# Performance work log

Hardware: AMD Instinct MI355X
Metric: run time of the kernel (lower is better)

## Reference

```python
import jax, jax.numpy as jnp
import numpy as np

NUM_HEADS = 32
NUM_KV_HEADS = 8
HEAD_DIM = 128
SEQ = 2048
MAX_SLOTS = 4096
SCALE = float(1.0 / np.sqrt(HEAD_DIM))  # attn_scale
G = NUM_HEADS // NUM_KV_HEADS  # num_queries_per_kv


def setup_inputs() -> dict:
    key = jax.random.key(0)
    k1, k2, k3 = jax.random.split(key, 3)
    q = jax.random.normal(k1, (SEQ, NUM_HEADS, HEAD_DIM), dtype=jnp.float32)
    k = jax.random.normal(k2, (SEQ, NUM_KV_HEADS, HEAD_DIM), dtype=jnp.float32)
    v = jax.random.normal(k3, (SEQ, NUM_KV_HEADS, HEAD_DIM), dtype=jnp.float32)
    k_cache = jnp.zeros((MAX_SLOTS, NUM_KV_HEADS, HEAD_DIM), dtype=jnp.float32)
    v_cache = jnp.zeros((MAX_SLOTS, NUM_KV_HEADS, HEAD_DIM), dtype=jnp.float32)
    slot_mapping = jnp.arange(SEQ, dtype=jnp.int64)  # contiguous block_table slots
    return {"q": q, "k": k, "v": v, "k_cache": k_cache, "v_cache": v_cache,
            "slot_mapping": slot_mapping}


def reference(q, k, v, k_cache, v_cache, slot_mapping):
    # prefill: scatter-write new K/V into the paged cache (self.k_cache[slot_mapping] = k)
    kc = k_cache.at[slot_mapping].set(k)
    vc = v_cache.at[slot_mapping].set(v)
    # gather K/V back from the cache via slot mapping (paged gather pattern)
    k_attn = kc[slot_mapping]  # (S, Hkv, D) == k since slots are unique
    v_attn = vc[slot_mapping]
    # GQA: repeat_interleave kv heads to match query heads
    kr = jnp.repeat(k_attn, G, axis=1)  # (S, H, D)
    vr = jnp.repeat(v_attn, G, axis=1)
    # scores: (H, Sq, Sk), naive full materialization as in the original
    scores = jnp.einsum('qhd,khd->hqk', q, kr) * SCALE
    sq, sk = q.shape[0], k_attn.shape[0]
    mask = jnp.tril(jnp.ones((sq, sk), dtype=bool))  # causal (num_query_tokens > 1)
    scores = jnp.where(mask[None, :, :], scores, -jnp.inf)
    weights = jax.nn.softmax(scores, axis=-1)
    out = jnp.einsum('hqk,khd->qhd', weights, vr)  # (S, H, D)
    return out
```

## Files before the change

### kernel.cpp

```cpp
#include <hip/hip_runtime.h>
#include <hip/hip_bf16.h>

#define SEQ 2048
#define QSTR 4096
#define CSCALE 0.1275174364688796f

typedef __attribute__((ext_vector_type(8)))  short short8;
typedef __attribute__((ext_vector_type(4)))  float f32x4;
typedef __attribute__((ext_vector_type(16))) float f32x16;

union PF8 { unsigned u[4]; short8 s; };

__device__ __forceinline__ unsigned short f2bf(float f) {
    union { __hip_bfloat16 b; unsigned short u; } cv;
    cv.b = __float2bfloat16(f);
    return cv.u;
}

__device__ __forceinline__ void gload16(const unsigned short* g, unsigned short* l) {
    __builtin_amdgcn_global_load_lds(
        (const __attribute__((address_space(1))) void*)g,
        (__attribute__((address_space(3))) void*)l, 16, 0, 0);
}

__global__ void prep_k(const float* __restrict__ Kg, unsigned short* __restrict__ Kb) {
    int gi = blockIdx.x * 256 + threadIdx.x;
    int kv = gi >> 8;
    int rem = gi & 255;
    int hk = rem >> 5;
    int d4 = rem & 31;
    f32x4 k4 = *(const f32x4*)(Kg + ((size_t)kv * 8 + hk) * 128 + 4 * d4);
    ushort4 u = make_ushort4(f2bf(k4[0]), f2bf(k4[1]), f2bf(k4[2]), f2bf(k4[3]));
    *(ushort4*)(Kb + ((size_t)hk * SEQ + kv) * 128 + 4 * d4) = u;
}

__global__ void prep_v(const float* __restrict__ Vg, unsigned short* __restrict__ Vtb) {
    const int hk  = blockIdx.x >> 5;
    const int kvb = blockIdx.x & 31;
    __shared__ unsigned short T[128][72];
    const int t = threadIdx.x;
    #pragma unroll
    for (int i = 0; i < 8; ++i) {
        int idx = t + 256 * i;
        int r = idx >> 5, d4 = idx & 31;
        f32x4 v = *(const f32x4*)(Vg + ((size_t)(kvb * 64 + r) * 8 + hk) * 128 + 4 * d4);
        T[4 * d4 + 0][r] = f2bf(v[0]);
        T[4 * d4 + 1][r] = f2bf(v[1]);
        T[4 * d4 + 2][r] = f2bf(v[2]);
        T[4 * d4 + 3][r] = f2bf(v[3]);
    }
    __syncthreads();
    #pragma unroll
    for (int i = 0; i < 8; ++i) {
        int idx = t + 256 * i;
        int d = idx >> 4, c4 = idx & 15;
        ushort4 u = *(ushort4*)&T[d][4 * c4];
        *(ushort4*)(Vtb + ((size_t)hk * 128 + d) * SEQ + kvb * 64 + 4 * c4) = u;
    }
}

__launch_bounds__(512, 2)
__global__ void attn_fwd(const float* __restrict__ Qg,
                         const unsigned short* __restrict__ Kb,
                         const unsigned short* __restrict__ Vtb,
                         float* __restrict__ Og) {
    const int bid = blockIdx.x;
    const int pr  = bid >> 5;
    const int h   = bid & 31;
    const int hk  = h >> 2;
    const int QBb = 15 - pr;
    const int QBa = pr;
    const int nsB = QBb + 1;

    const int tid  = threadIdx.x;
    const int w    = tid >> 6;
    const int wq   = w & 3;
    const int wk   = w >> 2;
    const int lane = tid & 63;
    const int q5   = lane & 31;
    const int t5   = lane >> 5;

    __shared__ __align__(16) unsigned char smem[150016];
    typedef unsigned short TileT[128][128];
    TileT* Ks = (TileT*)smem;
    TileT* Vt = (TileT*)(smem + 65536);
    float* mlm = (float*)(smem + 131072);
    float* mll = (float*)(smem + 132096);
    float (*Ot)[132] = (float(*)[132])(smem + 133120);

    short8 qf[8];
    auto LOADQ = [&](int QB) __attribute__((always_inline)) {
        const float* qp = Qg + (size_t)(QB * 128 + 32 * wq + q5) * QSTR + h * 128 + 8 * t5;
        #pragma unroll
        for (int st = 0; st < 8; ++st) {
            f32x4 a = *(const f32x4*)(qp + 16 * st);
            f32x4 b = *(const f32x4*)(qp + 16 * st + 4);
            short8 f;
            f[0] = (short)f2bf(a[0] * CSCALE); f[1] = (short)f2bf(a[1] * CSCALE);
            f[2] = (short)f2bf(a[2] * CSCALE); f[3] = (short)f2bf(a[3] * CSCALE);
            f[4] = (short)f2bf(b[0] * CSCALE); f[5] = (short)f2bf(b[1] * CSCALE);
            f[6] = (short)f2bf(b[2] * CSCALE); f[7] = (short)f2bf(b[3] * CSCALE);
            qf[st] = f;
        }
    };

    auto ISSUE = [&](int kv0, int b) __attribute__((always_inline)) {
        #pragma unroll
        for (int p4 = 0; p4 < 4; ++p4) {
            int row = 16 * w + 4 * p4 + (lane >> 4);
            const unsigned short* g = Kb +
                ((size_t)hk * SEQ + kv0 + row) * 128 + 8 * ((lane & 15) ^ (row & 15));
            gload16(g, &Ks[b][16 * w + 4 * p4][0]);
        }
        #pragma unroll
        for (int p4 = 0; p4 < 4; ++p4) {
            int row16 = 16 * w + 4 * p4 + (lane >> 4);
            int hh = row16 >> 6, r = row16 & 63;
            int gg = lane & 15;
            int d  = 2 * r + (gg >> 3);
            int c  = (gg & 7) ^ (r & 7);
            const unsigned short* g = Vtb +
                ((size_t)hk * 128 + d) * SEQ + kv0 + 64 * hh + 8 * c;
            gload16(g, &Vt[b][16 * w + 4 * p4][0]);
        }
    };

    f32x16 oacc[4];
    float m, l;
    auto RESET = [&]() __attribute__((always_inline)) {
        #pragma unroll
        for (int dt = 0; dt < 4; ++dt)
            #pragma unroll
            for (int r = 0; r < 16; ++r) oacc[dt][r] = 0.f;
        m = -1e30f; l = 0.f;
    };

    auto EPI = [&](int QBp) __attribute__((always_inline)) {
        if (t5 == 0) mlm[w * 32 + q5] = m;
        asm volatile("s_waitcnt lgkmcnt(0)" ::: "memory");
        __builtin_amdgcn_sched_barrier(0);
        __builtin_amdgcn_s_barrier();
        const float mOth = mlm[(w ^ 4) * 32 + q5];
        const float M  = fmaxf(m, mOth);
        const float sc = exp2f(m - M);
        const float lp = l * sc;
        #pragma unroll
        for (int dt = 0; dt < 4; ++dt)
            #pragma unroll
            for (int r = 0; r < 16; ++r) oacc[dt][r] *= sc;
        if (t5 == 0) mll[w * 32 + q5] = lp;
        asm volatile("s_waitcnt lgkmcnt(0)" ::: "memory");
        __builtin_amdgcn_sched_barrier(0);
        __builtin_amdgcn_s_barrier();
        const float lOth = mll[(w ^ 4) * 32 + q5];

        #pragma unroll 1
        for (int tq = 0; tq < 4; ++tq) {
            if (w == tq + 4) {
                #pragma unroll
                for (int dt = 0; dt < 4; ++dt)
                    #pragma unroll
                    for (int b = 0; b < 4; ++b) {
                        f32x4 v;
                        v[0] = oacc[dt][4 * b + 0]; v[1] = oacc[dt][4 * b + 1];
                        v[2] = oacc[dt][4 * b + 2]; v[3] = oacc[dt][4 * b + 3];
                        *(f32x4*)&Ot[q5][32 * dt + 8 * b + 4 * t5] = v;
                    }
            }
            asm volatile("s_waitcnt lgkmcnt(0)" ::: "memory");
            __builtin_amdgcn_sched_barrier(0);
            __builtin_amdgcn_s_barrier();
            if (w == tq) {
                const float rl = 1.0f / (lp + lOth);
                #pragma unroll
                for (int dt = 0; dt < 4; ++dt)
                    #pragma unroll
                    for (int b = 0; b < 4; ++b) {
                        f32x4 o1 = *(const f32x4*)&Ot[q5][32 * dt + 8 * b + 4 * t5];
                        f32x4 oc;
                        oc[0] = (oacc[dt][4 * b + 0] + o1[0]) * rl;
                        oc[1] = (oacc[dt][4 * b + 1] + o1[1]) * rl;
                        oc[2] = (oacc[dt][4 * b + 2] + o1[2]) * rl;
                        oc[3] = (oacc[dt][4 * b + 3] + o1[3]) * rl;
                        *(f32x4*)&Ot[q5][32 * dt + 8 * b + 4 * t5] = oc;
                    }
            }
            asm volatile("s_waitcnt lgkmcnt(0)" ::: "memory");
            __builtin_amdgcn_sched_barrier(0);
            __builtin_amdgcn_s_barrier();
            {
                float* ob = Og + (size_t)(QBp * 128 + 32 * tq) * QSTR + h * 128;
                #pragma unroll
                for (int i = 0; i < 2; ++i) {
                    int u  = tid + 512 * i;
                    int r  = u >> 5;
                    int c4 = (u & 31) * 4;
                    f32x4 v = *(const f32x4*)&Ot[r][c4];
                    *(f32x4*)(ob + (size_t)r * QSTR + c4) = v;
                }
            }
            asm volatile("s_waitcnt lgkmcnt(0)" ::: "memory");
            __builtin_amdgcn_sched_barrier(0);
            __builtin_amdgcn_s_barrier();
        }
    };

    LOADQ(QBb);
    #pragma unroll
    for (int st = 0; st < 8; ++st) asm volatile("" :: "v"(qf[st]));
    asm volatile("s_waitcnt vmcnt(0)" ::: "memory");
    RESET();

    ISSUE(0, 0);
    ISSUE(128, 1);

    for (int s = 0; s < 17; ++s) {
        if (s == nsB) {
            LOADQ(QBa);
            EPI(QBb);
            RESET();
        }
        const bool isB = (s < nsB);
        const int kv0   = isB ? 128 * s : 128 * (s - nsB);
        const int q0blk = isB ? 128 * QBb : 128 * QBa;
        const int buf = s & 1;

        if (s + 1 < 17) asm volatile("s_waitcnt vmcnt(8)" ::: "memory");
        else            asm volatile("s_waitcnt vmcnt(0)" ::: "memory");
        __builtin_amdgcn_s_barrier();

        const int q0w = q0blk + 32 * wq;
        const int kvb = kv0 + 64 * wk;
        if (kvb <= q0w + 31) {
            f32x16 sac[2];
            __builtin_amdgcn_s_setprio(1);
            #pragma unroll
            for (int kvs = 0; kvs < 2; ++kvs) {
                f32x16 acc;
                #pragma unroll
                for (int r = 0; r < 16; ++r) acc[r] = 0.f;
                #pragma unroll
                for (int st = 0; st < 8; ++st) {
                    short8 kf = *(const short8*)
                        &Ks[buf][64 * wk + 32 * kvs + q5][8 * ((2 * st + t5) ^ (q5 & 15))];
                    acc = __builtin_amdgcn_mfma_f32_32x32x16_bf16(kf, qf[st], acc, 0, 0, 0);
                }
                sac[kvs] = acc;
            }
            __builtin_amdgcn_s_setprio(0);

            if (kvb + 63 > q0w) {
                const int qrow = q0w + q5;
                #pragma unroll
                for (int kvs = 0; kvs < 2; ++kvs)
                    #pragma unroll
                    for (int r = 0; r < 16; ++r) {
                        int kv = kvb + 32 * kvs + (r & 3) + 8 * (r >> 2) + 4 * t5;
                        if (kv > qrow) sac[kvs][r] = -1e30f;
                    }
            }

            float t16[16], t8[8], t4[4], t2[2];
            #pragma unroll
            for (int i = 0; i < 16; ++i) t16[i] = fmaxf(sac[0][i], sac[1][i]);
            #pragma unroll
            for (int i = 0; i < 8; ++i) t8[i] = fmaxf(t16[i], t16[i + 8]);
            #pragma unroll
            for (int i = 0; i < 4; ++i) t4[i] = fmaxf(t8[i], t8[i + 4]);
            t2[0] = fmaxf(t4[0], t4[2]); t2[1] = fmaxf(t4[1], t4[3]);
            float mx = fmaxf(t2[0], t2[1]);
            mx = fmaxf(mx, __shfl_xor(mx, 32));

            const bool skip = __all(mx <= m + 11.0f);
            float fac = 1.0f;
            if (!skip) {
                float mn = fmaxf(m, mx);
                fac = exp2f(m - mn);
                m = mn;
            }

            float ps;
            {
                #pragma unroll
                for (int kvs = 0; kvs < 2; ++kvs)
                    #pragma unroll
                    for (int r = 0; r < 16; ++r)
                        sac[kvs][r] = exp2f(sac[kvs][r] - m);
                float s16[16], s8[8], s4[4], s2[2];
                #pragma unroll
                for (int i = 0; i < 16; ++i) s16[i] = sac[0][i] + sac[1][i];
                #pragma unroll
                for (int i = 0; i < 8; ++i) s8[i] = s16[i] + s16[i + 8];
                #pragma unroll
                for (int i = 0; i < 4; ++i) s4[i] = s8[i] + s8[i + 4];
                s2[0] = s4[0] + s4[2]; s2[1] = s4[1] + s4[3];
                ps = s2[0] + s2[1];
                ps += __shfl_xor(ps, 32);
            }
            if (!skip) {
                l = l * fac + ps;
                #pragma unroll
                for (int dt = 0; dt < 4; ++dt)
                    #pragma unroll
                    for (int r = 0; r < 16; ++r) oacc[dt][r] *= fac;
            } else {
                l += ps;
            }

            unsigned pkw[2][8];
            #pragma unroll
            for (int a = 0; a < 2; ++a)
                #pragma unroll
                for (int rp = 0; rp < 8; ++rp)
                    pkw[a][rp] = (unsigned)f2bf(sac[a][2 * rp]) |
                                 ((unsigned)f2bf(sac[a][2 * rp + 1]) << 16);

            unsigned rcv[2][4];
            #pragma unroll
            for (int a = 0; a < 2; ++a)
                #pragma unroll
                for (int i = 0; i < 4; ++i) {
                    const int loI = (i & 1) + 4 * (i >> 1);
                    const int hiI = loI + 2;
                    unsigned wsend = t5 ? pkw[a][loI] : pkw[a][hiI];
                    rcv[a][i] = (unsigned)__shfl_xor((int)wsend, 32);
                }

            PF8 pf[4];
            #pragma unroll
            for (int ks = 0; ks < 4; ++ks) {
                const int a = ks >> 1;
                #pragma unroll
                for (int j = 0; j < 4; ++j) {
                    const int ib = (j & 1) + 4 * (ks & 1);
                    const int ri = (j & 1) + 2 * (ks & 1);
                    const unsigned own_lo = pkw[a][ib];
                    const unsigned own_hi = pkw[a][ib + 2];
                    const unsigned par    = rcv[a][ri];
                    pf[ks].u[j] = (j < 2) ? (t5 ? par : own_lo)
                                          : (t5 ? own_hi : par);
                }
            }

            __builtin_amdgcn_s_setprio(1);
            #pragma unroll
            for (int dt = 0; dt < 4; ++dt) {
                #pragma unroll
                for (int ks = 0; ks < 4; ++ks) {
                    const int gg = 8 * (q5 & 1) +
                        ((2 * ks + t5) ^ ((q5 >> 1) & 7));
                    short8 vf = *(const short8*)
                        &Vt[buf][64 * wk + 16 * dt + (q5 >> 1)][8 * gg];
                    oacc[dt] = __builtin_amdgcn_mfma_f32_32x32x16_bf16(vf, pf[ks].s, oacc[dt], 0, 0, 0);
                }
            }
            __builtin_amdgcn_s_setprio(0);
        }

        asm volatile("" ::: "memory");
        __builtin_amdgcn_s_barrier();
        if (s + 2 < 17) {
            const int s2 = s + 2;
            ISSUE((s2 < nsB) ? 128 * s2 : 128 * (s2 - nsB), s & 1);
        }
    }

    EPI(QBa);
}

extern "C" void kernel_launch(void* const* d_in, const int* in_sizes, int n_in,
                              void* d_out, int out_size, void* d_ws, size_t ws_size,
                              hipStream_t stream) {
    const float* q = (const float*)d_in[0];
    const float* k = (const float*)d_in[1];
    const float* v = (const float*)d_in[2];
    float* out = (float*)d_out;
    unsigned short* Kb  = (unsigned short*)d_ws;
    unsigned short* Vtb = Kb + (size_t)8 * SEQ * 128;
    prep_k<<<dim3(2048), 256, 0, stream>>>(k, Kb);
    prep_v<<<dim3(256), 256, 0, stream>>>(v, Vtb);
    attn_fwd<<<dim3(256), 512, 0, stream>>>(q, Kb, Vtb, out);
}
```

Baseline: 87.15 us.

## Software-pipeline QK^T of next tile and prefetch V fragments into registers

Restructures the KV loop so each step computes the QK^T MFMAs for the next tile before running softmax and the PV product of the current tile. V fragments for the next tile are preloaded into registers, which takes LDS reads off the PV MFMA chain. The next-tile global loads are issued right after the step barrier instead of at the end of the step, and the second Q block is loaded one step early. The goal is to overlap MFMA work with softmax VALU work and LDS latency. The cost is much higher register pressure (two score accumulator sets plus 16 V fragments), which risks spills or lower occupancy, and a full vmcnt(0) wait at every step.

```diff
diff --git a/kernel.cpp b/kernel.cpp
--- a/kernel.cpp
+++ b/kernel.cpp
@@ -88,7 +88,10 @@
     float* mll = (float*)(smem + 132096);
     float (*Ot)[132] = (float(*)[132])(smem + 133120);
 
-    short8 qf[8];
+    short8 qf[8], vregC[16];
+    f32x16 oacc[4];
+    float m, l;
+
     auto LOADQ = [&](int QB) __attribute__((always_inline)) {
         const float* qp = Qg + (size_t)(QB * 128 + 32 * wq + q5) * QSTR + h * 128 + 8 * t5;
         #pragma unroll
@@ -125,8 +128,35 @@
         }
     };
 
-    f32x16 oacc[4];
-    float m, l;
+    auto QKT = [&](int bb, f32x16 (&out)[2]) __attribute__((always_inline)) {
+        __builtin_amdgcn_s_setprio(1);
+        #pragma unroll
+        for (int kvs = 0; kvs < 2; ++kvs) {
+            f32x16 acc;
+            #pragma unroll
+            for (int r = 0; r < 16; ++r) acc[r] = 0.f;
+            #pragma unroll
+            for (int st = 0; st < 8; ++st) {
+                short8 kf = *(const short8*)
+                    &Ks[bb][64 * wk + 32 * kvs + q5][8 * ((2 * st + t5) ^ (q5 & 15))];
+                acc = __builtin_amdgcn_mfma_f32_32x32x16_bf16(kf, qf[st], acc, 0, 0, 0);
+            }
+            out[kvs] = acc;
+        }
+        __builtin_amdgcn_s_setprio(0);
+    };
+
+    auto RFV = [&](int bb) __attribute__((always_inline)) {
+        #pragma unroll
+        for (int dt = 0; dt < 4; ++dt)
+            #pragma unroll
+            for (int ks = 0; ks < 4; ++ks) {
+                const int gg = 8 * (q5 & 1) + ((2 * ks + t5) ^ ((q5 >> 1) & 7));
+                vregC[4 * dt + ks] = *(const short8*)
+                    &Vt[bb][64 * wk + 16 * dt + (q5 >> 1)][8 * gg];
+            }
+    };
+
     auto RESET = [&]() __attribute__((always_inline)) {
         #pragma unroll
         for (int dt = 0; dt < 4; ++dt)
@@ -205,50 +235,35 @@
         }
     };
 
-    LOADQ(QBb);
-    #pragma unroll
-    for (int st = 0; st < 8; ++st) asm volatile("" :: "v"(qf[st]));
-    asm volatile("s_waitcnt vmcnt(0)" ::: "memory");
-    RESET();
-
-    ISSUE(0, 0);
-    ISSUE(128, 1);
-
-    for (int s = 0; s < 17; ++s) {
-        if (s == nsB) {
-            LOADQ(QBa);
-            EPI(QBb);
-            RESET();
-        }
-        const bool isB = (s < nsB);
-        const int kv0   = isB ? 128 * s : 128 * (s - nsB);
-        const int q0blk = isB ? 128 * QBb : 128 * QBa;
-        const int buf = s & 1;
-
-        if (s + 1 < 17) asm volatile("s_waitcnt vmcnt(8)" ::: "memory");
-        else            asm volatile("s_waitcnt vmcnt(0)" ::: "memory");
+    auto STEP = [&](f32x16 (&sacCur)[2], f32x16 (&sacNxt)[2], int s)
+        __attribute__((always_inline)) {
+        asm volatile("s_waitcnt vmcnt(0) lgkmcnt(0)" ::: "memory");
+        __builtin_amdgcn_sched_barrier(0);
         __builtin_amdgcn_s_barrier();
 
-        const int q0w = q0blk + 32 * wq;
-        const int kvb = kv0 + 64 * wk;
+        if (s == nsB - 1) LOADQ(QBa);
+        if (s == nsB) { EPI(QBb); RESET(); }
+
+        if (s + 2 < 17) {
+            const int x = s + 2;
+            ISSUE((x < nsB) ? 128 * x : 128 * (x - nsB), s & 1);
+        }
+
+        const int t1 = s + 1;
+        bool act1 = false;
+        if (t1 < 17) {
+            const bool iB = t1 < nsB;
+            const int kv0n = iB ? 128 * t1 : 128 * (t1 - nsB);
+            const int q0n  = (iB ? QBb : QBa) * 128 + 32 * wq;
+            act1 = (kv0n + 64 * wk) <= q0n + 31;
+        }
+        if (act1) QKT(t1 & 1, sacNxt);
+
+        const bool iBt = s < nsB;
+        const int kv0t = iBt ? 128 * s : 128 * (s - nsB);
+        const int q0w  = (iBt ? QBb : QBa) * 128 + 32 * wq;
+        const int kvb  = kv0t + 64 * wk;
         if (kvb <= q0w + 31) {
-            f32x16 sac[2];
-            __builtin_amdgcn_s_setprio(1);
-            #pragma unroll
-            for (int kvs = 0; kvs < 2; ++kvs) {
-                f32x16 acc;
-                #pragma unroll
-                for (int r = 0; r < 16; ++r) acc[r] = 0.f;
-                #pragma unroll
-                for (int st = 0; st < 8; ++st) {
-                    short8 kf = *(const short8*)
-                        &Ks[buf][64 * wk + 32 * kvs + q5][8 * ((2 * st + t5) ^ (q5 & 15))];
-                    acc = __builtin_amdgcn_mfma_f32_32x32x16_bf16(kf, qf[st], acc, 0, 0, 0);
-                }
-                sac[kvs] = acc;
-            }
-            __builtin_amdgcn_s_setprio(0);
-
             if (kvb + 63 > q0w) {
                 const int qrow = q0w + q5;
                 #pragma unroll
@@ -256,13 +271,12 @@
                     #pragma unroll
                     for (int r = 0; r < 16; ++r) {
                         int kv = kvb + 32 * kvs + (r & 3) + 8 * (r >> 2) + 4 * t5;
-                        if (kv > qrow) sac[kvs][r] = -1e30f;
+                        if (kv > qrow) sacCur[kvs][r] = -1e30f;
                     }
             }
-
             float t16[16], t8[8], t4[4], t2[2];
             #pragma unroll
-            for (int i = 0; i < 16; ++i) t16[i] = fmaxf(sac[0][i], sac[1][i]);
+            for (int i = 0; i < 16; ++i) t16[i] = fmaxf(sacCur[0][i], sacCur[1][i]);
             #pragma unroll
             for (int i = 0; i < 8; ++i) t8[i] = fmaxf(t16[i], t16[i + 8]);
             #pragma unroll
@@ -278,17 +292,16 @@
                 fac = exp2f(m - mn);
                 m = mn;
             }
-
             float ps;
             {
                 #pragma unroll
                 for (int kvs = 0; kvs < 2; ++kvs)
                     #pragma unroll
                     for (int r = 0; r < 16; ++r)
-                        sac[kvs][r] = exp2f(sac[kvs][r] - m);
+                        sacCur[kvs][r] = exp2f(sacCur[kvs][r] - m);
                 float s16[16], s8[8], s4[4], s2[2];
                 #pragma unroll
-                for (int i = 0; i < 16; ++i) s16[i] = sac[0][i] + sac[1][i];
+                for (int i = 0; i < 16; ++i) s16[i] = sacCur[0][i] + sacCur[1][i];
                 #pragma unroll
                 for (int i = 0; i < 8; ++i) s8[i] = s16[i] + s16[i + 8];
                 #pragma unroll
@@ -312,8 +325,8 @@
             for (int a = 0; a < 2; ++a)
                 #pragma unroll
                 for (int rp = 0; rp < 8; ++rp)
-                    pkw[a][rp] = (unsigned)f2bf(sac[a][2 * rp]) |
-                                 ((unsigned)f2bf(sac[a][2 * rp + 1]) << 16);
+                    pkw[a][rp] = (unsigned)f2bf(sacCur[a][2 * rp]) |
+                                 ((unsigned)f2bf(sacCur[a][2 * rp + 1]) << 16);
 
             unsigned rcv[2][4];
             #pragma unroll
@@ -344,26 +357,37 @@
 
             __builtin_amdgcn_s_setprio(1);
             #pragma unroll
-            for (int dt = 0; dt < 4; ++dt) {
-                #pragma unroll
-                for (int ks = 0; ks < 4; ++ks) {
-                    const int gg = 8 * (q5 & 1) +
-                        ((2 * ks + t5) ^ ((q5 >> 1) & 7));
-                    short8 vf = *(const short8*)
-                        &Vt[buf][64 * wk + 16 * dt + (q5 >> 1)][8 * gg];
-                    oacc[dt] = __builtin_amdgcn_mfma_f32_32x32x16_bf16(vf, pf[ks].s, oacc[dt], 0, 0, 0);
-                }
-            }
+            for (int dt = 0; dt < 4; ++dt)
+                #pragma unroll
+                for (int ks = 0; ks < 4; ++ks)
+                    oacc[dt] = __builtin_amdgcn_mfma_f32_32x32x16_bf16(
+                        vregC[4 * dt + ks], pf[ks].s, oacc[dt], 0, 0, 0);
             __builtin_amdgcn_s_setprio(0);
         }
 
-        asm volatile("" ::: "memory");
-        __builtin_amdgcn_s_barrier();
-        if (s + 2 < 17) {
-            const int s2 = s + 2;
-            ISSUE((s2 < nsB) ? 128 * s2 : 128 * (s2 - nsB), s & 1);
-        }
+        if (act1) RFV(t1 & 1);
+    };
+
+    LOADQ(QBb);
+    #pragma unroll
+    for (int st = 0; st < 8; ++st) asm volatile("" :: "v"(qf[st]));
+    asm volatile("s_waitcnt vmcnt(0)" ::: "memory");
+    RESET();
+    ISSUE(0, 0);
+    ISSUE(128, 1);
+    asm volatile("s_waitcnt vmcnt(0)" ::: "memory");
+    __builtin_amdgcn_s_barrier();
+
+    f32x16 sacA[2], sacB[2];
+    QKT(0, sacA);
+    RFV(0);
+
+    #pragma unroll 1
+    for (int s2 = 0; s2 < 8; ++s2) {
+        STEP(sacA, sacB, 2 * s2);
+        STEP(sacB, sacA, 2 * s2 + 1);
     }
+    STEP(sacA, sacB, 16);
 
     EPI(QBa);
 }
```

Result: slower. 239.5 us (+174.8%).
